# Kernel tuning notes

Measured on AMD Instinct MI355X. Metric: run time of the kernel, lower is better.

Reference implementation:

```python
import jax, jax.numpy as jnp
import numpy as np

HEAD_SIZE = 20
NUM_HEADS = 2


def setup_inputs() -> dict:
    key = jax.random.key(0)
    k1, k2, k3, k4, k5, k6 = jax.random.split(key, 6)
    N, L, D = 32, 256, HEAD_SIZE
    x = jax.random.normal(k1, (N, N, L, D), dtype=jnp.float32)
    y = jax.random.normal(k2, (N, N, L, D), dtype=jnp.float32)
    s = 1.0 / np.sqrt(D)
    WQ = jax.random.normal(k3, (D, HEAD_SIZE * NUM_HEADS), dtype=jnp.float32) * s
    WK = jax.random.normal(k4, (D, HEAD_SIZE * NUM_HEADS), dtype=jnp.float32) * s
    WV = jax.random.normal(k5, (D, HEAD_SIZE * NUM_HEADS), dtype=jnp.float32) * s
    WH = jax.random.normal(k6, (HEAD_SIZE * NUM_HEADS, HEAD_SIZE), dtype=jnp.float32) * s
    return {"x": x, "y": y, "WQ": WQ, "WK": WK, "WV": WV, "WH": WH}


def _masked_softmax(logits):
    # mask wherever the raw logit is exactly zero (custom zero-value mask)
    mask = logits != 0
    z = jnp.exp(logits - jnp.max(logits, axis=-1, keepdims=True))
    z = jnp.where(mask, z, jnp.zeros_like(z))
    return z / (jnp.sum(z, axis=-1, keepdims=True) + 1e-10)


def reference(x, y, WQ, WK, WV, WH):
    nSet_x, nSet_y, Lx, D = x.shape
    Ly = y.shape[2]
    H, Dh = NUM_HEADS, HEAD_SIZE
    scale = 1.0 / jnp.sqrt(jnp.asarray(Dh, dtype=jnp.float32))

    # cross branch: transpose x [1,0,2,3] then flatten set dims
    xq = jnp.transpose(x, (1, 0, 2, 3)).reshape(-1, Lx, D)  # [B, Lx, D]
    yf = y.reshape(-1, Ly, D)                               # [B, Ly, D]

    q = xq @ WQ   # [B, Lx, H*Dh]
    k = yf @ WK   # [B, Ly, H*Dh]
    v = yf @ WV   # [B, Ly, H*Dh]

    B = q.shape[0]
    q = q.reshape(B, Lx, H, Dh).transpose(0, 2, 1, 3)  # [B, H, Lx, Dh]
    k = k.reshape(B, Ly, H, Dh).transpose(0, 2, 1, 3)
    v = v.reshape(B, Ly, H, Dh).transpose(0, 2, 1, 3)

    logits = jnp.einsum('bhqd,bhkd->bhqk', q, k) * scale  # [B, H, Lx, Ly]
    attn = _masked_softmax(logits)
    o = jnp.einsum('bhqk,bhkd->bhqd', attn, v)            # [B, H, Lx, Dh]
    o = o.transpose(0, 2, 1, 3).reshape(B, Lx, H * Dh)
    out = o @ WH                                          # [B, Lx, Dh]

    out = out.reshape(nSet_x, nSet_y, Lx, Dh).transpose(1, 0, 2, 3)
    return out
```

## Files before the change

kernel.cpp:

```cpp
#include <hip/hip_runtime.h>
#include <stdint.h>


#define NSET 32
#define SEQL 256
#define DM   20
#define NH   2
#define DH   20

typedef __attribute__((ext_vector_type(8))) short short8;
typedef __attribute__((ext_vector_type(4))) short short4v;
typedef __attribute__((ext_vector_type(4))) float f32x4;

#define MFMA32(a, b, c) __builtin_amdgcn_mfma_f32_16x16x32_bf16((a), (b), (c), 0, 0, 0)

#if __has_builtin(__builtin_amdgcn_mfma_f32_16x16x16bf16_1k)
#define MFMA16(a, b, c) __builtin_amdgcn_mfma_f32_16x16x16bf16_1k((a), (b), (c), 0, 0, 0)
#elif __has_builtin(__builtin_amdgcn_mfma_f32_16x16x16_bf16)
#define MFMA16(a, b, c) __builtin_amdgcn_mfma_f32_16x16x16_bf16((a), (b), (c), 0, 0, 0)
#else
static __device__ __forceinline__ f32x4 MFMA16(short4v a, short4v b, f32x4 c) {
    asm volatile("s_nop 1\n\tv_mfma_f32_16x16x16_bf16 %0, %1, %2, %0\n\ts_nop 7"
                 : "+v"(c) : "v"(a), "v"(b));
    return c;
}
#endif

__device__ __forceinline__ uint32_t bfhu(float f) {
    return (__float_as_uint(f) + 0x8000u) >> 16;
}
__device__ __forceinline__ uint32_t packbf(float hi, float lo) {
    return __builtin_amdgcn_perm(__float_as_uint(hi) + 0x8000u,
                                 __float_as_uint(lo) + 0x8000u, 0x07060302u);
}
__device__ __forceinline__ float fexp2(float x) {
    float r;
    asm("v_exp_f32 %0, %1" : "=v"(r) : "v"(x));
    return r;
}

__device__ __forceinline__ short8 ldsA(const short* base, int row, int qd) {
    short8 f = {0, 0, 0, 0, 0, 0, 0, 0};
    if (qd < 3) f = *(const short8*)(base + row * 24 + qd * 8);
    return f;
}

__device__ __forceinline__ short8 gfrag(const float* rowp, int qd) {
    short8 f = {0, 0, 0, 0, 0, 0, 0, 0};
    if (qd < 2) {
        float4 a = *(const float4*)(rowp + qd * 8);
        float4 b = *(const float4*)(rowp + qd * 8 + 4);
        f[0] = (short)bfhu(a.x); f[1] = (short)bfhu(a.y);
        f[2] = (short)bfhu(a.z); f[3] = (short)bfhu(a.w);
        f[4] = (short)bfhu(b.x); f[5] = (short)bfhu(b.y);
        f[6] = (short)bfhu(b.z); f[7] = (short)bfhu(b.w);
    } else if (qd == 2) {
        float4 a = *(const float4*)(rowp + 16);
        f[0] = (short)bfhu(a.x); f[1] = (short)bfhu(a.y);
        f[2] = (short)bfhu(a.z); f[3] = (short)bfhu(a.w);
    }
    return f;
}

#define SMEM_BYTES 47744

__global__ __launch_bounds__(512, 4) void set_attn_v11(
    const float* __restrict__ x, const float* __restrict__ y,
    const float* __restrict__ wq, const float* __restrict__ wk,
    const float* __restrict__ wv, const float* __restrict__ wh,
    float* __restrict__ out)
{
    __shared__ __align__(16) char smem[SMEM_BYTES];
    short* sKb  = (short*)smem;
    short* sVtb = (short*)(smem + 24576);
    float* sL   = (float*)(smem + 45696);
    float* sOut = (float*)smem;

    const int tid     = threadIdx.x;
    const int lane    = tid & 63;
    const int w       = tid >> 6;
    const int c       = lane & 15;
    const int qd      = lane >> 4;
    const int head    = w >> 2;
    const int rowbase = (w & 3) * 64;
    const int b       = blockIdx.x;
    const int bi      = b >> 5, bj = b & 31;

    short* sK  = sKb + head * (SEQL * 24);
    short* sVt = sVtb + head * (20 * 264);
    short* myO = sKb + w * (64 * 24);

    *(uint2*)(sKb + tid * 24 + 20) = make_uint2(0u, 0u);

    const float QS = 0.22360679774997896f * 1.4426950408889634f;

    short8 xf[4];
#pragma unroll
    for (int mt = 0; mt < 4; ++mt)
        xf[mt] = gfrag(x + ((size_t)b * SEQL + rowbase + mt * 16 + c) * DM, qd);

    short8 wqA0 = {0,0,0,0,0,0,0,0}, wqA1 = wqA0;
#pragma unroll
    for (int j = 0; j < 8; ++j) {
        int k = qd * 8 + j;
        if (k < 20) {
            wqA0[j] = (short)bfhu(wq[k * 40 + head * 20 + c]);
            if (c < 4) wqA1[j] = (short)bfhu(wq[k * 40 + head * 20 + 16 + c]);
        }
    }

    short8 wkf[2], wvf[2];
#pragma unroll
    for (int dt = 0; dt < 2; ++dt) {
        int n = dt * 16 + c;
        short8 fk = {0,0,0,0,0,0,0,0}, fv = fk;
        if (n < 20) {
#pragma unroll
            for (int j = 0; j < 8; ++j) {
                int k = qd * 8 + j;
                if (k < 20) {
                    fk[j] = (short)bfhu(wk[k * 40 + head * 20 + n]);
                    fv[j] = (short)bfhu(wv[k * 40 + head * 20 + n]);
                }
            }
        }
        wkf[dt] = fk; wvf[dt] = fv;
    }

    const int i01 = (c + ((qd & 1) << 5)) << 2;
    const int i23 = (c + 16 + ((qd & 1) << 5)) << 2;
    const int iB  = c << 2;

    short8 qb[4];
#pragma unroll
    for (int mt = 0; mt < 4; ++mt) {
        int rb = rowbase + mt * 16;
        short8 yf = gfrag(y + ((size_t)(bj * NSET + bi) * SEQL + rb + c) * DM, qd);
#pragma unroll
        for (int dt = 0; dt < 2; ++dt) {
            f32x4 z = {0.f, 0.f, 0.f, 0.f};
            f32x4 kres = MFMA32(yf, wkf[dt], z);
            f32x4 vres = MFMA32(yf, wvf[dt], z);
            int n = dt * 16 + c;
            if (n < 20) {
#pragma unroll
                for (int reg = 0; reg < 4; ++reg)
                    sK[(rb + qd * 4 + reg) * 24 + n] = (short)bfhu(kres[reg]);
                uint2 pv = make_uint2(packbf(vres[1], vres[0]),
                                      packbf(vres[3], vres[2]));
                *(uint2*)(sVt + n * 264 + rb + qd * 4) = pv;
            }
        }
        {
            f32x4 z = {0.f, 0.f, 0.f, 0.f};
            f32x4 ra = MFMA32(wqA0, xf[mt], z);
            f32x4 rb2 = MFMA32(wqA1, xf[mt], z);
            uint32_t dwA0 = packbf(ra[1] * QS, ra[0] * QS);
            uint32_t dwA1 = packbf(ra[3] * QS, ra[2] * QS);
            uint32_t dwB0 = packbf(rb2[1] * QS, rb2[0] * QS);
            uint32_t dwB1 = packbf(rb2[3] * QS, rb2[2] * QS);
            uint32_t t0a = (uint32_t)__builtin_amdgcn_ds_bpermute(i01, (int)dwA0);
            uint32_t t1a = (uint32_t)__builtin_amdgcn_ds_bpermute(i01, (int)dwA1);
            uint32_t t0b = (uint32_t)__builtin_amdgcn_ds_bpermute(iB, (int)dwB0);
            uint32_t t1b = (uint32_t)__builtin_amdgcn_ds_bpermute(iB, (int)dwB1);
            uint32_t t2  = (uint32_t)__builtin_amdgcn_ds_bpermute(i23, (int)dwA0);
            uint32_t t3  = (uint32_t)__builtin_amdgcn_ds_bpermute(i23, (int)dwA1);
            uint32_t q0 = qd < 2 ? t0a : (qd == 2 ? t0b : 0u);
            uint32_t q1 = qd < 2 ? t1a : (qd == 2 ? t1b : 0u);
            uint32_t q2 = qd < 2 ? t2 : 0u;
            uint32_t q3 = qd < 2 ? t3 : 0u;
            short8 f;
            *(uint2*)&f = make_uint2(q0, q1);
            *(((uint2*)&f) + 1) = make_uint2(q2, q3);
            qb[mt] = f;
        }
    }
    __syncthreads();

    f32x4 oacc[4][2];
#pragma unroll
    for (int mt = 0; mt < 4; ++mt)
#pragma unroll
        for (int dt = 0; dt < 2; ++dt) oacc[mt][dt] = (f32x4){0.f, 0.f, 0.f, 0.f};
    float ls0 = 0.f, ls1 = 0.f, ls2 = 0.f, ls3 = 0.f;

    for (int s0 = 0; s0 < SEQL; s0 += 32) {
        short8 kf0 = ldsA(sK, s0 + c, qd);
        short8 kf1 = ldsA(sK, s0 + 16 + c, qd);
        short4v vb[2][2];
#pragma unroll
        for (int dt = 0; dt < 2; ++dt) {
            int d = dt * 16 + c;
#pragma unroll
            for (int st = 0; st < 2; ++st) {
                uint2 u = make_uint2(0u, 0u);
                if (d < 20)
                    u = *(const uint2*)(sVt + d * 264 + s0 + st * 16 + qd * 4);
                short4v t; *(uint2*)&t = u;
                vb[st][dt] = t;
            }
        }
#pragma unroll
        for (int mt = 0; mt < 4; ++mt) {
#pragma unroll
            for (int st = 0; st < 2; ++st) {
                f32x4 z = {0.f, 0.f, 0.f, 0.f};
                f32x4 sacc = MFMA32((st == 0 ? kf0 : kf1), qb[mt], z);
                float p0, p1, p2, p3;
                {
                    float v0 = sacc[0], v1 = sacc[1], v2 = sacc[2], v3 = sacc[3];
                    p0 = (v0 != 0.f) ? fexp2(v0) : 0.f;
                    p1 = (v1 != 0.f) ? fexp2(v1) : 0.f;
                    p2 = (v2 != 0.f) ? fexp2(v2) : 0.f;
                    p3 = (v3 != 0.f) ? fexp2(v3) : 0.f;
                }
                float lsum = (p0 + p1) + (p2 + p3);
                if (mt == 0) ls0 += lsum;
                else if (mt == 1) ls1 += lsum;
                else if (mt == 2) ls2 += lsum;
                else ls3 += lsum;
                short4v pf;
                *(uint2*)&pf = make_uint2(packbf(p1, p0), packbf(p3, p2));
                oacc[mt][0] = MFMA16(pf, vb[st][0], oacc[mt][0]);
                oacc[mt][1] = MFMA16(pf, vb[st][1], oacc[mt][1]);
            }
        }
    }

    ls0 += __shfl_xor(ls0, 16, 64); ls0 += __shfl_xor(ls0, 32, 64);
    ls1 += __shfl_xor(ls1, 16, 64); ls1 += __shfl_xor(ls1, 32, 64);
    ls2 += __shfl_xor(ls2, 16, 64); ls2 += __shfl_xor(ls2, 32, 64);
    ls3 += __shfl_xor(ls3, 16, 64); ls3 += __shfl_xor(ls3, 32, 64);
    float sel = ls0;
    if (qd == 1) sel = ls1;
    if (qd == 2) sel = ls2;
    if (qd == 3) sel = ls3;
    sL[w * 64 + lane] = sel;
    __syncthreads();

    short8 whf[2];
#pragma unroll
    for (int dt = 0; dt < 2; ++dt) {
        int n = dt * 16 + c;
        short8 f = {0,0,0,0,0,0,0,0};
        if (n < 20) {
#pragma unroll
            for (int j = 0; j < 8; ++j) {
                int k = qd * 8 + j;
                if (k < 20) f[j] = (short)bfhu(wh[(head * 20 + k) * 20 + n]);
            }
        }
        whf[dt] = f;
    }
#pragma unroll
    for (int mt = 0; mt < 4; ++mt) {
        float inv[4];
#pragma unroll
        for (int reg = 0; reg < 4; ++reg)
            inv[reg] = 1.f / (sL[w * 64 + mt * 16 + qd * 4 + reg] + 1e-10f);
#pragma unroll
        for (int dt = 0; dt < 2; ++dt) {
            int n = dt * 16 + c;
            if (n < 20) {
#pragma unroll
                for (int reg = 0; reg < 4; ++reg)
                    myO[(mt * 16 + qd * 4 + reg) * 24 + n] =
                        (short)bfhu(oacc[mt][dt][reg] * inv[reg]);
            }
        }
    }
    __syncthreads();

    f32x4 outacc[4][2];
#pragma unroll
    for (int mt = 0; mt < 4; ++mt) {
        short8 of = ldsA(myO, mt * 16 + c, qd);
        f32x4 z = {0.f, 0.f, 0.f, 0.f};
        outacc[mt][0] = MFMA32(of, whf[0], z);
        outacc[mt][1] = MFMA32(of, whf[1], z);
    }
    __syncthreads();

    if (head == 1) {
#pragma unroll
        for (int mt = 0; mt < 4; ++mt)
#pragma unroll
            for (int dt = 0; dt < 2; ++dt) {
                int n = dt * 16 + c;
                if (n < 20) {
#pragma unroll
                    for (int reg = 0; reg < 4; ++reg) {
                        int row = rowbase + mt * 16 + qd * 4 + reg;
                        sOut[row * 20 + n] = outacc[mt][dt][reg];
                    }
                }
            }
    }
    __syncthreads();

    if (head == 0) {
        float* ob = out + (size_t)b * (SEQL * DH);
#pragma unroll
        for (int mt = 0; mt < 4; ++mt)
#pragma unroll
            for (int dt = 0; dt < 2; ++dt) {
                int n = dt * 16 + c;
                if (n < 20) {
#pragma unroll
                    for (int reg = 0; reg < 4; ++reg) {
                        int row = rowbase + mt * 16 + qd * 4 + reg;
                        ob[row * 20 + n] = outacc[mt][dt][reg] + sOut[row * 20 + n];
                    }
                }
            }
    }
}

extern "C" void kernel_launch(void* const* d_in, const int* in_sizes, int n_in,
                              void* d_out, int out_size, void* d_ws, size_t ws_size,
                              hipStream_t stream) {
    const float* x  = (const float*)d_in[0];
    const float* y  = (const float*)d_in[1];
    const float* wq = (const float*)d_in[2];
    const float* wk = (const float*)d_in[3];
    const float* wv = (const float*)d_in[4];
    const float* wh = (const float*)d_in[5];
    float* out = (float*)d_out;

    set_attn_v11<<<dim3(NSET * NSET), dim3(512), 0, stream>>>(x, y, wq, wk, wv, wh, out);
}
```

Before: 147.3 us.

## Compact LDS layouts to stride 20, XOR-swizzle V^T, shuffle row sums

Shrinks the K and output tiles in shared memory from a padded row stride of 24 to 20 shorts, and stores V-transposed at a stride of 256 with an XOR swizzle to avoid bank conflicts. The softmax row sums are now broadcast with wave shuffles instead of a shared-memory array. LDS use per block drops so more blocks can be resident, at the cost of split 8-byte loads and more shuffle instructions. K-fragment loads now read 8-byte pieces without padding, so alignment and bank conflict behavior changes.

```diff
diff --git a/kernel.cpp b/kernel.cpp
--- a/kernel.cpp
+++ b/kernel.cpp
@@ -39,10 +39,19 @@
     return r;
 }
 
-__device__ __forceinline__ short8 ldsA(const short* base, int row, int qd) {
-    short8 f = {0, 0, 0, 0, 0, 0, 0, 0};
-    if (qd < 3) f = *(const short8*)(base + row * 24 + qd * 8);
+__device__ __forceinline__ short8 ldsA20(const short* base, int row, int qd) {
+    uint2 lo = make_uint2(0u, 0u), hi = make_uint2(0u, 0u);
+    const short* p = base + row * 20 + qd * 8;
+    if (qd < 2) { lo = *(const uint2*)p; hi = *(const uint2*)(p + 4); }
+    else if (qd == 2) { lo = *(const uint2*)p; }
+    short8 f;
+    *(uint2*)&f = lo;
+    *(((uint2*)&f) + 1) = hi;
     return f;
+}
+
+__device__ __forceinline__ int vtoff(int d, int s) {
+    return d * 256 + (s ^ ((d & 7) << 2));
 }
 
 __device__ __forceinline__ short8 gfrag(const float* rowp, int qd) {
@@ -62,9 +71,9 @@
     return f;
 }
 
-#define SMEM_BYTES 47744
-
-__global__ __launch_bounds__(512, 4) void set_attn_v11(
+#define SMEM_BYTES 40960
+
+__global__ __launch_bounds__(512, 4) void set_attn_v12(
     const float* __restrict__ x, const float* __restrict__ y,
     const float* __restrict__ wq, const float* __restrict__ wk,
     const float* __restrict__ wv, const float* __restrict__ wh,
@@ -72,8 +81,7 @@
 {
     __shared__ __align__(16) char smem[SMEM_BYTES];
     short* sKb  = (short*)smem;
-    short* sVtb = (short*)(smem + 24576);
-    float* sL   = (float*)(smem + 45696);
+    short* sVtb = (short*)(smem + 20480);
     float* sOut = (float*)smem;
 
     const int tid     = threadIdx.x;
@@ -86,11 +94,9 @@
     const int b       = blockIdx.x;
     const int bi      = b >> 5, bj = b & 31;
 
-    short* sK  = sKb + head * (SEQL * 24);
-    short* sVt = sVtb + head * (20 * 264);
-    short* myO = sKb + w * (64 * 24);
-
-    *(uint2*)(sKb + tid * 24 + 20) = make_uint2(0u, 0u);
+    short* sK  = sKb + head * (SEQL * 20);
+    short* sVt = sVtb + head * (20 * 256);
+    short* myO = sKb + w * (64 * 20);
 
     const float QS = 0.22360679774997896f * 1.4426950408889634f;
 
@@ -145,10 +151,10 @@
             if (n < 20) {
 #pragma unroll
                 for (int reg = 0; reg < 4; ++reg)
-                    sK[(rb + qd * 4 + reg) * 24 + n] = (short)bfhu(kres[reg]);
+                    sK[(rb + qd * 4 + reg) * 20 + n] = (short)bfhu(kres[reg]);
                 uint2 pv = make_uint2(packbf(vres[1], vres[0]),
                                       packbf(vres[3], vres[2]));
-                *(uint2*)(sVt + n * 264 + rb + qd * 4) = pv;
+                *(uint2*)(sVt + vtoff(n, rb + qd * 4)) = pv;
             }
         }
         {
@@ -185,8 +191,8 @@
     float ls0 = 0.f, ls1 = 0.f, ls2 = 0.f, ls3 = 0.f;
 
     for (int s0 = 0; s0 < SEQL; s0 += 32) {
-        short8 kf0 = ldsA(sK, s0 + c, qd);
-        short8 kf1 = ldsA(sK, s0 + 16 + c, qd);
+        short8 kf0 = ldsA20(sK, s0 + c, qd);
+        short8 kf1 = ldsA20(sK, s0 + 16 + c, qd);
         short4v vb[2][2];
 #pragma unroll
         for (int dt = 0; dt < 2; ++dt) {
@@ -195,7 +201,7 @@
             for (int st = 0; st < 2; ++st) {
                 uint2 u = make_uint2(0u, 0u);
                 if (d < 20)
-                    u = *(const uint2*)(sVt + d * 264 + s0 + st * 16 + qd * 4);
+                    u = *(const uint2*)(sVt + vtoff(d, s0 + st * 16 + qd * 4));
                 short4v t; *(uint2*)&t = u;
                 vb[st][dt] = t;
             }
@@ -231,11 +237,6 @@
     ls1 += __shfl_xor(ls1, 16, 64); ls1 += __shfl_xor(ls1, 32, 64);
     ls2 += __shfl_xor(ls2, 16, 64); ls2 += __shfl_xor(ls2, 32, 64);
     ls3 += __shfl_xor(ls3, 16, 64); ls3 += __shfl_xor(ls3, 32, 64);
-    float sel = ls0;
-    if (qd == 1) sel = ls1;
-    if (qd == 2) sel = ls2;
-    if (qd == 3) sel = ls3;
-    sL[w * 64 + lane] = sel;
     __syncthreads();
 
     short8 whf[2];
@@ -254,17 +255,18 @@
     }
 #pragma unroll
     for (int mt = 0; mt < 4; ++mt) {
+        float lsm = (mt == 0) ? ls0 : (mt == 1) ? ls1 : (mt == 2) ? ls2 : ls3;
         float inv[4];
 #pragma unroll
         for (int reg = 0; reg < 4; ++reg)
-            inv[reg] = 1.f / (sL[w * 64 + mt * 16 + qd * 4 + reg] + 1e-10f);
+            inv[reg] = 1.f / (__shfl(lsm, qd * 4 + reg, 64) + 1e-10f);
 #pragma unroll
         for (int dt = 0; dt < 2; ++dt) {
             int n = dt * 16 + c;
             if (n < 20) {
 #pragma unroll
                 for (int reg = 0; reg < 4; ++reg)
-                    myO[(mt * 16 + qd * 4 + reg) * 24 + n] =
+                    myO[(mt * 16 + qd * 4 + reg) * 20 + n] =
                         (short)bfhu(oacc[mt][dt][reg] * inv[reg]);
             }
         }
@@ -274,7 +276,7 @@
     f32x4 outacc[4][2];
 #pragma unroll
     for (int mt = 0; mt < 4; ++mt) {
-        short8 of = ldsA(myO, mt * 16 + c, qd);
+        short8 of = ldsA20(myO, mt * 16 + c, qd);
         f32x4 z = {0.f, 0.f, 0.f, 0.f};
         outacc[mt][0] = MFMA32(of, whf[0], z);
         outacc[mt][1] = MFMA32(of, whf[1], z);
@@ -327,5 +329,5 @@
     const float* wh = (const float*)d_in[5];
     float* out = (float*)d_out;
 
-    set_attn_v11<<<dim3(NSET * NSET), dim3(512), 0, stream>>>(x, y, wq, wk, wv, wh, out);
-}
+    set_attn_v12<<<dim3(NSET * NSET), dim3(512), 0, stream>>>(x, y, wq, wk, wv, wh, out);
+}
```

New measurement: 146.9 us. Within noise of the previous version (-0.3%).
